# Kernel tuning notes

Measured on AMD Instinct MI355X. Metric: run time of the kernel, lower is better.

## Reference

```python
import jax, jax.numpy as jnp
import numpy as np

B = 256   # batch size; must equal N for the module's final broadcast to be valid
N = 256   # num feature vectors per sample
D = 1024  # feature dim
S = 1024  # state dim


def setup_inputs() -> dict:
    key = jax.random.key(0)
    k1, k2, k3, k4 = jax.random.split(key, 4)
    return {
        "feature_vectors": jax.random.normal(k1, (B, N, D), dtype=jnp.float32),
        "state_output": jax.random.normal(k2, (B, S), dtype=jnp.float32),
        # tf.random_normal_initializer default stddev=0.05
        "Q": 0.05 * jax.random.normal(k3, (S, S), dtype=jnp.float32),
        "K": 0.05 * jax.random.normal(k4, (S, N), dtype=jnp.float32),
    }


def reference(feature_vectors, state_output, Q, K):
    # Loop body: ((Q @ state^T)^T @ K) @ feature_vectors[i]
    # (Q @ state^T)^T == state @ Q^T  -> [B, S]
    A = state_output @ Q.T            # [B, S]
    M = A @ K                         # [B, N]
    # stack over i: W[i, b, d] = sum_n M[b, n] * FV[i, n, d]
    W = jnp.einsum('bn,ind->ibd', M, feature_vectors)   # [B, B, D]
    W = jax.nn.softmax(W, axis=-1)
    # broadcast multiply [B, B, D] * [B, N(=B), D], sum over axis=1
    context_vector = jnp.sum(W * feature_vectors, axis=1)  # [B, D]
    return (context_vector, W)
```

## Files before the change

### kernel.cpp

```cpp
#include <hip/hip_runtime.h>


typedef _Float16 half8 __attribute__((ext_vector_type(8)));
typedef _Float16 half4 __attribute__((ext_vector_type(4)));
typedef float floatx16 __attribute__((ext_vector_type(16)));

static __device__ __forceinline__ void split_f32(float x, _Float16& hi, _Float16& lo) {
    _Float16 h = (_Float16)x;
    hi = h;
    lo = (_Float16)(x - (float)h);
}

template <bool BT>
__global__ __launch_bounds__(256, 2) void gemm_splitk(
    const float* __restrict__ Ag, const float* __restrict__ Bg,
    float* __restrict__ Cf, int Kdim, int Ndim, int KC)
{
    __shared__ __align__(16) _Float16 AsHi[4 * 64 * 8];
    __shared__ __align__(16) _Float16 AsLo[4 * 64 * 8];
    __shared__ __align__(16) _Float16 BsHi[4 * 64 * 8];
    __shared__ __align__(16) _Float16 BsLo[4 * 64 * 8];

    const int tid  = threadIdx.x;
    const int lane = tid & 63;
    const int wave = tid >> 6;
    const int wy = wave >> 1, wx = wave & 1;
    const int l31 = lane & 31, l5 = lane >> 5;
    const int m0 = blockIdx.y * 64, n0 = blockIdx.x * 64;
    const int kt0 = (blockIdx.z * KC) >> 5;

    floatx16 acc;
#pragma unroll
    for (int j = 0; j < 16; ++j) acc[j] = 0.0f;

    const int sA_m  = tid >> 2;
    const int sA_kg = tid & 3;
    const int sB_n  = tid & 63;
    const int sB_kg = tid >> 6;

    const int nkt = KC / 32;
#pragma unroll 1
    for (int kt2 = 0; kt2 < nkt; ++kt2) {
        const int kt = kt0 + kt2;
        __syncthreads();
        {
            const float* src = Ag + (size_t)(m0 + sA_m) * Kdim + kt * 32 + sA_kg * 8;
            half8 hi, lo;
#pragma unroll
            for (int j = 0; j < 8; ++j) {
                _Float16 h, l;
                split_f32(src[j], h, l);
                hi[j] = h; lo[j] = l;
            }
            *(half8*)&AsHi[(sA_kg * 64 + sA_m) * 8] = hi;
            *(half8*)&AsLo[(sA_kg * 64 + sA_m) * 8] = lo;
        }
        if constexpr (BT) {
            const float* src = Bg + (size_t)(n0 + sA_m) * Kdim + kt * 32 + sA_kg * 8;
            half8 hi, lo;
#pragma unroll
            for (int j = 0; j < 8; ++j) {
                _Float16 h, l;
                split_f32(src[j], h, l);
                hi[j] = h; lo[j] = l;
            }
            *(half8*)&BsHi[(sA_kg * 64 + sA_m) * 8] = hi;
            *(half8*)&BsLo[(sA_kg * 64 + sA_m) * 8] = lo;
        } else {
            const float* src = Bg + (size_t)(kt * 32 + sB_kg * 8) * Ndim + n0 + sB_n;
            half8 hi, lo;
#pragma unroll
            for (int j = 0; j < 8; ++j) {
                _Float16 h, l;
                split_f32(src[(size_t)j * Ndim], h, l);
                hi[j] = h; lo[j] = l;
            }
            *(half8*)&BsHi[(sB_kg * 64 + sB_n) * 8] = hi;
            *(half8*)&BsLo[(sB_kg * 64 + sB_n) * 8] = lo;
        }
        __syncthreads();
#pragma unroll
        for (int ks = 0; ks < 2; ++ks) {
            const int kg = ks * 2 + l5;
            const half8 ah = *(half8*)&AsHi[(kg * 64 + wy * 32 + l31) * 8];
            const half8 al = *(half8*)&AsLo[(kg * 64 + wy * 32 + l31) * 8];
            const half8 bh = *(half8*)&BsHi[(kg * 64 + wx * 32 + l31) * 8];
            const half8 bl = *(half8*)&BsLo[(kg * 64 + wx * 32 + l31) * 8];
            acc = __builtin_amdgcn_mfma_f32_32x32x16_f16(ah, bh, acc, 0, 0, 0);
            acc = __builtin_amdgcn_mfma_f32_32x32x16_f16(ah, bl, acc, 0, 0, 0);
            acc = __builtin_amdgcn_mfma_f32_32x32x16_f16(al, bh, acc, 0, 0, 0);
        }
    }

#pragma unroll
    for (int reg = 0; reg < 16; ++reg) {
        const int row = m0 + wy * 32 + (reg & 3) + 8 * (reg >> 2) + 4 * l5;
        const int col = n0 + wx * 32 + l31;
        atomicAdd(&Cf[(size_t)row * Ndim + col], acc[reg]);
    }
}

static __device__ __forceinline__ int bs_swz(int byte_off) {
    return byte_off ^ (((byte_off >> 7) & 7) << 4);
}

__global__ __launch_bounds__(1024, 4) void fused_attn(
    const float* __restrict__ FV, const float* __restrict__ Mf,
    float* __restrict__ ctx, float* __restrict__ Wout)
{
    __shared__ __align__(16) _Float16 AsHi[2 * 64 * 8];
    __shared__ __align__(16) _Float16 AsLo[2 * 64 * 8];
    __shared__ __align__(16) _Float16 Bs[2 * 1024 * 8];
    __shared__ __align__(16) float red1[64 * 8];
    __shared__ __align__(16) float red2[64 * 8];

    const int tid  = threadIdx.x;
    const int lane = tid & 63;
    const int wave = tid >> 6;
    const int wx = wave & 7;
    const int wy = wave >> 3;
    const int l31 = lane & 31, l5 = lane >> 5;

    const int w   = blockIdx.x;
    const int xcd = w & 7;
    const int k   = w >> 3;
    const int i   = (xcd << 5) + (k >> 2);
    const int bt  = k & 3;

    const float* __restrict__ FVi = FV + (size_t)i * 256 * 1024;

    floatx16 acc[4];
#pragma unroll
    for (int nt = 0; nt < 4; ++nt)
#pragma unroll
        for (int j = 0; j < 16; ++j) acc[nt][j] = 0.0f;

    const int am = tid >> 1, akg = tid & 1;

    const int ng = tid >> 8;
    const int dq = tid & 255;

    float4 pv[4];
    float4 pa0, pa1;
#pragma unroll
    for (int r = 0; r < 4; ++r)
        pv[r] = *(const float4*)(FVi + (size_t)(ng * 4 + r) * 1024 + dq * 4);
    if (tid < 128) {
        const float* ap = Mf + (size_t)(bt * 64 + am) * 256 + akg * 8;
        pa0 = *(const float4*)(ap);
        pa1 = *(const float4*)(ap + 4);
    }

#pragma unroll 1
    for (int kt = 0; kt < 16; ++kt) {
        __syncthreads();
        if (tid < 128) {
            half8 hi, lo;
#pragma unroll
            for (int j = 0; j < 4; ++j) {
                _Float16 h, l;
                split_f32((&pa0.x)[j], h, l);
                hi[j] = h; lo[j] = l;
            }
#pragma unroll
            for (int j = 0; j < 4; ++j) {
                _Float16 h, l;
                split_f32((&pa1.x)[j], h, l);
                hi[4 + j] = h; lo[4 + j] = l;
            }
            *(half8*)&AsHi[(akg * 64 + am) * 8] = hi;
            *(half8*)&AsLo[(akg * 64 + am) * 8] = lo;
        }
#pragma unroll
        for (int j = 0; j < 4; ++j) {
            half4 h;
#pragma unroll
            for (int r = 0; r < 4; ++r) h[r] = (_Float16)((&pv[r].x)[j]);
            const int byte_off = ((ng >> 1) * 1024 + dq * 4 + j) * 16 + (ng & 1) * 8;
            *(half4*)((char*)Bs + bs_swz(byte_off)) = h;
        }
        __syncthreads();
        if (kt + 1 < 16) {
#pragma unroll
            for (int r = 0; r < 4; ++r)
                pv[r] = *(const float4*)(FVi + (size_t)((kt + 1) * 16 + ng * 4 + r) * 1024 + dq * 4);
            if (tid < 128) {
                const float* ap = Mf + (size_t)(bt * 64 + am) * 256 + (kt + 1) * 16 + akg * 8;
                pa0 = *(const float4*)(ap);
                pa1 = *(const float4*)(ap + 4);
            }
        }
        const half8 ah = *(half8*)&AsHi[(l5 * 64 + wy * 32 + l31) * 8];
        const half8 al = *(half8*)&AsLo[(l5 * 64 + wy * 32 + l31) * 8];
#pragma unroll
        for (int nt = 0; nt < 4; ++nt) {
            const int byte_off = (l5 * 1024 + wx * 128 + nt * 32 + l31) * 16;
            const half8 b = *(const half8*)((const char*)Bs + bs_swz(byte_off));
            acc[nt] = __builtin_amdgcn_mfma_f32_32x32x16_f16(ah, b, acc[nt], 0, 0, 0);
            acc[nt] = __builtin_amdgcn_mfma_f32_32x32x16_f16(al, b, acc[nt], 0, 0, 0);
        }
    }

#pragma unroll
    for (int reg = 0; reg < 16; ++reg) {
        float v = acc[0][reg];
#pragma unroll
        for (int nt = 1; nt < 4; ++nt) v = fmaxf(v, acc[nt][reg]);
#pragma unroll
        for (int off = 1; off < 32; off <<= 1) v = fmaxf(v, __shfl_xor(v, off));
        if (l31 == 0) {
            const int row = wy * 32 + (reg & 3) + 8 * (reg >> 2) + 4 * l5;
            red1[row * 8 + wx] = v;
        }
    }
    __syncthreads();
#pragma unroll
    for (int reg = 0; reg < 16; ++reg) {
        const int row = wy * 32 + (reg & 3) + 8 * (reg >> 2) + 4 * l5;
        const float4 a4 = *(const float4*)&red1[row * 8];
        const float4 b4 = *(const float4*)&red1[row * 8 + 4];
        const float rmax = fmaxf(fmaxf(fmaxf(a4.x, a4.y), fmaxf(a4.z, a4.w)),
                                 fmaxf(fmaxf(b4.x, b4.y), fmaxf(b4.z, b4.w)));
        float s = 0.0f;
#pragma unroll
        for (int nt = 0; nt < 4; ++nt) {
            const float p = __expf(acc[nt][reg] - rmax);
            acc[nt][reg] = p;
            s += p;
        }
#pragma unroll
        for (int off = 1; off < 32; off <<= 1) s += __shfl_xor(s, off);
        if (l31 == 0) red2[row * 8 + wx] = s;
    }
    __syncthreads();

    float csum[4];
#pragma unroll
    for (int nt = 0; nt < 4; ++nt) csum[nt] = 0.0f;

    const int rowbase = bt * 64 + wy * 32;
#pragma unroll
    for (int reg = 0; reg < 16; ++reg) {
        const int row = (reg & 3) + 8 * (reg >> 2) + 4 * l5;
        const float4 a4 = *(const float4*)&red2[(wy * 32 + row) * 8];
        const float4 b4 = *(const float4*)&red2[(wy * 32 + row) * 8 + 4];
        const float inv = 1.0f / (a4.x + a4.y + a4.z + a4.w + b4.x + b4.y + b4.z + b4.w);
#pragma unroll
        for (int nt = 0; nt < 4; ++nt) {
            const int col = wx * 128 + nt * 32 + l31;
            const float wv = acc[nt][reg] * inv;
            Wout[((size_t)(i * 256 + rowbase + row)) * 1024 + col] = wv;
            const float fv = FVi[(size_t)(rowbase + row) * 1024 + col];
            csum[nt] += wv * fv;
        }
    }
#pragma unroll
    for (int nt = 0; nt < 4; ++nt) {
        const float v = csum[nt] + __shfl_xor(csum[nt], 32);
        if (l5 == 0)
            atomicAdd(&ctx[(size_t)i * 1024 + wx * 128 + nt * 32 + l31], v);
    }
}

extern "C" void kernel_launch(void* const* d_in, const int* in_sizes, int n_in,
                              void* d_out, int out_size, void* d_ws, size_t ws_size,
                              hipStream_t stream)
{
    const float* FV    = (const float*)d_in[0];
    const float* state = (const float*)d_in[1];
    const float* Q     = (const float*)d_in[2];
    const float* Km    = (const float*)d_in[3];

    float* out = (float*)d_out;
    float* ctx = out;
    float* W   = out + 256 * 1024;

    char* ws = (char*)d_ws;
    float* A1 = (float*)ws;
    float* Mf = (float*)(ws + (1 << 20));

    (void)hipMemsetAsync(ws, 0, (1 << 20) + (1 << 18), stream);
    (void)hipMemsetAsync(ctx, 0, 256 * 1024 * sizeof(float), stream);

    gemm_splitk<true><<<dim3(16, 4, 8), 256, 0, stream>>>(
        state, Q, A1, 1024, 1024, 128);

    gemm_splitk<false><<<dim3(4, 4, 16), 256, 0, stream>>>(
        A1, Km, Mf, 1024, 256, 64);

    fused_attn<<<dim3(1024), 1024, 0, stream>>>(FV, Mf, ctx, W);
}
```

Measured before the change: 585.7 us.

## Split fused attention into two D-sliced passes with cross-slice softmax stats

Replaces the single fused kernel (one block per 64 rows over full D) with two launches where each block covers all 256 rows for a 256-wide D slice. Pass 1 computes per-slice row max and exp-sum into workspace. Pass 2 recomputes the GEMM, merges the slice statistics, and writes normalized W and the context sum using the FV slice cached in LDS. This cuts redundant FV reads and reuses the staged FV tile for the context product, but recomputes the GEMM and runs with large LDS and low occupancy.

After: 727.1 us. 1.24x slower.

```diff
diff --git a/kernel.cpp b/kernel.cpp
--- a/kernel.cpp
+++ b/kernel.cpp
@@ -2,7 +2,6 @@
 
 
 typedef _Float16 half8 __attribute__((ext_vector_type(8)));
-typedef _Float16 half4 __attribute__((ext_vector_type(4)));
 typedef float floatx16 __attribute__((ext_vector_type(16)));
 
 static __device__ __forceinline__ void split_f32(float x, _Float16& hi, _Float16& lo) {
@@ -100,165 +99,169 @@
     }
 }
 
-static __device__ __forceinline__ int bs_swz(int byte_off) {
-    return byte_off ^ (((byte_off >> 7) & 7) << 4);
-}
-
-__global__ __launch_bounds__(1024, 4) void fused_attn(
+static __device__ __forceinline__ int swz5(int byte_off) {
+    return byte_off ^ (((byte_off >> 9) & 31) << 4);
+}
+
+template <int PASS>
+__global__ __launch_bounds__(512, 1) void pass_k(
     const float* __restrict__ FV, const float* __restrict__ Mf,
+    float* __restrict__ Sm, float* __restrict__ Ss,
     float* __restrict__ ctx, float* __restrict__ Wout)
 {
-    __shared__ __align__(16) _Float16 AsHi[2 * 64 * 8];
-    __shared__ __align__(16) _Float16 AsLo[2 * 64 * 8];
-    __shared__ __align__(16) _Float16 Bs[2 * 1024 * 8];
-    __shared__ __align__(16) float red1[64 * 8];
-    __shared__ __align__(16) float red2[64 * 8];
+    __shared__ __align__(16) _Float16 Bs[256 * 256];
+    __shared__ __align__(16) float redm[256 * 2];
+    __shared__ __align__(16) float reds[256 * 2];
 
     const int tid  = threadIdx.x;
     const int lane = tid & 63;
     const int wave = tid >> 6;
-    const int wx = wave & 7;
-    const int wy = wave >> 3;
+    const int wy   = wave >> 1;
+    const int wx   = wave & 1;
     const int l31 = lane & 31, l5 = lane >> 5;
 
-    const int w   = blockIdx.x;
-    const int xcd = w & 7;
-    const int k   = w >> 3;
-    const int i   = (xcd << 5) + (k >> 2);
-    const int bt  = k & 3;
-
-    const float* __restrict__ FVi = FV + (size_t)i * 256 * 1024;
-
-    floatx16 acc[4];
-#pragma unroll
-    for (int nt = 0; nt < 4; ++nt)
-#pragma unroll
-        for (int j = 0; j < 16; ++j) acc[nt][j] = 0.0f;
-
-    const int am = tid >> 1, akg = tid & 1;
-
-    const int ng = tid >> 8;
-    const int dq = tid & 255;
-
-    float4 pv[4];
-    float4 pa0, pa1;
-#pragma unroll
-    for (int r = 0; r < 4; ++r)
-        pv[r] = *(const float4*)(FVi + (size_t)(ng * 4 + r) * 1024 + dq * 4);
-    if (tid < 128) {
-        const float* ap = Mf + (size_t)(bt * 64 + am) * 256 + akg * 8;
-        pa0 = *(const float4*)(ap);
-        pa1 = *(const float4*)(ap + 4);
-    }
+    const int i  = blockIdx.x >> 2;
+    const int ds = blockIdx.x & 3;
+
+    const float* __restrict__ FVi = FV + (size_t)i * 262144 + ds * 256;
+
+    floatx16 acc[8];
+#pragma unroll
+    for (int t = 0; t < 8; ++t)
+#pragma unroll
+        for (int j = 0; j < 16; ++j) acc[t][j] = 0.0f;
+
+    const int sd  = tid & 255;
+    const int snh = tid >> 8;
+
+    const float* __restrict__ Ar0 = Mf + (size_t)(wy * 64 + l31) * 256 + l5 * 8;
+    const float* __restrict__ Ar1 = Mf + (size_t)(wy * 64 + 32 + l31) * 256 + l5 * 8;
+
+    float pv[8];
+#pragma unroll
+    for (int r = 0; r < 8; ++r)
+        pv[r] = FVi[(size_t)(snh * 8 + r) * 1024 + sd];
 
 #pragma unroll 1
     for (int kt = 0; kt < 16; ++kt) {
-        __syncthreads();
-        if (tid < 128) {
-            half8 hi, lo;
+        {
+            half8 h;
+#pragma unroll
+            for (int r = 0; r < 8; ++r) h[r] = (_Float16)pv[r];
+            const int byte_off = sd * 512 + (kt * 16 + snh * 8) * 2;
+            *(half8*)((char*)Bs + swz5(byte_off)) = h;
+        }
+        __syncthreads();
+        if (kt + 1 < 16) {
+#pragma unroll
+            for (int r = 0; r < 8; ++r)
+                pv[r] = FVi[(size_t)((kt + 1) * 16 + snh * 8 + r) * 1024 + sd];
+        }
+        half8 ah0, al0, ah1, al1;
+        {
+            const float4 x0 = *(const float4*)(Ar0 + kt * 16);
+            const float4 x1 = *(const float4*)(Ar0 + kt * 16 + 4);
+            const float4 y0 = *(const float4*)(Ar1 + kt * 16);
+            const float4 y1 = *(const float4*)(Ar1 + kt * 16 + 4);
 #pragma unroll
             for (int j = 0; j < 4; ++j) {
                 _Float16 h, l;
-                split_f32((&pa0.x)[j], h, l);
-                hi[j] = h; lo[j] = l;
-            }
-#pragma unroll
-            for (int j = 0; j < 4; ++j) {
-                _Float16 h, l;
-                split_f32((&pa1.x)[j], h, l);
-                hi[4 + j] = h; lo[4 + j] = l;
-            }
-            *(half8*)&AsHi[(akg * 64 + am) * 8] = hi;
-            *(half8*)&AsLo[(akg * 64 + am) * 8] = lo;
-        }
-#pragma unroll
-        for (int j = 0; j < 4; ++j) {
-            half4 h;
-#pragma unroll
-            for (int r = 0; r < 4; ++r) h[r] = (_Float16)((&pv[r].x)[j]);
-            const int byte_off = ((ng >> 1) * 1024 + dq * 4 + j) * 16 + (ng & 1) * 8;
-            *(half4*)((char*)Bs + bs_swz(byte_off)) = h;
-        }
-        __syncthreads();
-        if (kt + 1 < 16) {
-#pragma unroll
-            for (int r = 0; r < 4; ++r)
-                pv[r] = *(const float4*)(FVi + (size_t)((kt + 1) * 16 + ng * 4 + r) * 1024 + dq * 4);
-            if (tid < 128) {
-                const float* ap = Mf + (size_t)(bt * 64 + am) * 256 + (kt + 1) * 16 + akg * 8;
-                pa0 = *(const float4*)(ap);
-                pa1 = *(const float4*)(ap + 4);
-            }
-        }
-        const half8 ah = *(half8*)&AsHi[(l5 * 64 + wy * 32 + l31) * 8];
-        const half8 al = *(half8*)&AsLo[(l5 * 64 + wy * 32 + l31) * 8];
-#pragma unroll
-        for (int nt = 0; nt < 4; ++nt) {
-            const int byte_off = (l5 * 1024 + wx * 128 + nt * 32 + l31) * 16;
-            const half8 b = *(const half8*)((const char*)Bs + bs_swz(byte_off));
-            acc[nt] = __builtin_amdgcn_mfma_f32_32x32x16_f16(ah, b, acc[nt], 0, 0, 0);
-            acc[nt] = __builtin_amdgcn_mfma_f32_32x32x16_f16(al, b, acc[nt], 0, 0, 0);
-        }
-    }
-
-#pragma unroll
-    for (int reg = 0; reg < 16; ++reg) {
-        float v = acc[0][reg];
-#pragma unroll
-        for (int nt = 1; nt < 4; ++nt) v = fmaxf(v, acc[nt][reg]);
-#pragma unroll
-        for (int off = 1; off < 32; off <<= 1) v = fmaxf(v, __shfl_xor(v, off));
-        if (l31 == 0) {
-            const int row = wy * 32 + (reg & 3) + 8 * (reg >> 2) + 4 * l5;
-            red1[row * 8 + wx] = v;
-        }
-    }
-    __syncthreads();
-#pragma unroll
-    for (int reg = 0; reg < 16; ++reg) {
-        const int row = wy * 32 + (reg & 3) + 8 * (reg >> 2) + 4 * l5;
-        const float4 a4 = *(const float4*)&red1[row * 8];
-        const float4 b4 = *(const float4*)&red1[row * 8 + 4];
-        const float rmax = fmaxf(fmaxf(fmaxf(a4.x, a4.y), fmaxf(a4.z, a4.w)),
-                                 fmaxf(fmaxf(b4.x, b4.y), fmaxf(b4.z, b4.w)));
-        float s = 0.0f;
-#pragma unroll
-        for (int nt = 0; nt < 4; ++nt) {
-            const float p = __expf(acc[nt][reg] - rmax);
-            acc[nt][reg] = p;
-            s += p;
-        }
-#pragma unroll
-        for (int off = 1; off < 32; off <<= 1) s += __shfl_xor(s, off);
-        if (l31 == 0) red2[row * 8 + wx] = s;
-    }
-    __syncthreads();
-
-    float csum[4];
-#pragma unroll
-    for (int nt = 0; nt < 4; ++nt) csum[nt] = 0.0f;
-
-    const int rowbase = bt * 64 + wy * 32;
-#pragma unroll
-    for (int reg = 0; reg < 16; ++reg) {
-        const int row = (reg & 3) + 8 * (reg >> 2) + 4 * l5;
-        const float4 a4 = *(const float4*)&red2[(wy * 32 + row) * 8];
-        const float4 b4 = *(const float4*)&red2[(wy * 32 + row) * 8 + 4];
-        const float inv = 1.0f / (a4.x + a4.y + a4.z + a4.w + b4.x + b4.y + b4.z + b4.w);
-#pragma unroll
-        for (int nt = 0; nt < 4; ++nt) {
-            const int col = wx * 128 + nt * 32 + l31;
-            const float wv = acc[nt][reg] * inv;
-            Wout[((size_t)(i * 256 + rowbase + row)) * 1024 + col] = wv;
-            const float fv = FVi[(size_t)(rowbase + row) * 1024 + col];
-            csum[nt] += wv * fv;
-        }
-    }
-#pragma unroll
-    for (int nt = 0; nt < 4; ++nt) {
-        const float v = csum[nt] + __shfl_xor(csum[nt], 32);
-        if (l5 == 0)
-            atomicAdd(&ctx[(size_t)i * 1024 + wx * 128 + nt * 32 + l31], v);
+                split_f32((&x0.x)[j], h, l); ah0[j] = h;     al0[j] = l;
+                split_f32((&x1.x)[j], h, l); ah0[4 + j] = h; al0[4 + j] = l;
+                split_f32((&y0.x)[j], h, l); ah1[j] = h;     al1[j] = l;
+                split_f32((&y1.x)[j], h, l); ah1[4 + j] = h; al1[4 + j] = l;
+            }
+        }
+#pragma unroll
+        for (int dt = 0; dt < 4; ++dt) {
+            const int byte_off = (wx * 128 + dt * 32 + l31) * 512 + (kt * 16 + l5 * 8) * 2;
+            const half8 b = *(const half8*)((const char*)Bs + swz5(byte_off));
+            acc[dt]     = __builtin_amdgcn_mfma_f32_32x32x16_f16(ah0, b, acc[dt], 0, 0, 0);
+            acc[dt]     = __builtin_amdgcn_mfma_f32_32x32x16_f16(al0, b, acc[dt], 0, 0, 0);
+            acc[4 + dt] = __builtin_amdgcn_mfma_f32_32x32x16_f16(ah1, b, acc[4 + dt], 0, 0, 0);
+            acc[4 + dt] = __builtin_amdgcn_mfma_f32_32x32x16_f16(al1, b, acc[4 + dt], 0, 0, 0);
+        }
+    }
+
+    if constexpr (PASS == 1) {
+#pragma unroll
+        for (int mt = 0; mt < 2; ++mt)
+#pragma unroll
+            for (int reg = 0; reg < 16; ++reg) {
+                float v = fmaxf(fmaxf(acc[mt * 4 + 0][reg], acc[mt * 4 + 1][reg]),
+                                fmaxf(acc[mt * 4 + 2][reg], acc[mt * 4 + 3][reg]));
+#pragma unroll
+                for (int off = 1; off < 32; off <<= 1) v = fmaxf(v, __shfl_xor(v, off));
+                if (l31 == 0) {
+                    const int row = wy * 64 + mt * 32 + (reg & 3) + 8 * (reg >> 2) + 4 * l5;
+                    redm[row * 2 + wx] = v;
+                }
+            }
+        __syncthreads();
+#pragma unroll
+        for (int mt = 0; mt < 2; ++mt)
+#pragma unroll
+            for (int reg = 0; reg < 16; ++reg) {
+                const int row = wy * 64 + mt * 32 + (reg & 3) + 8 * (reg >> 2) + 4 * l5;
+                const float m = fmaxf(redm[row * 2], redm[row * 2 + 1]);
+                float s = 0.0f;
+#pragma unroll
+                for (int dt = 0; dt < 4; ++dt) s += __expf(acc[mt * 4 + dt][reg] - m);
+#pragma unroll
+                for (int off = 1; off < 32; off <<= 1) s += __shfl_xor(s, off);
+                if (l31 == 0) reds[row * 2 + wx] = s;
+            }
+        __syncthreads();
+        if (tid < 256) {
+            const int b = tid;
+            const float m = fmaxf(redm[b * 2], redm[b * 2 + 1]);
+            const float s = reds[b * 2] + reds[b * 2 + 1];
+            const int sidx = (i * 4 + ds) * 256 + b;
+            Sm[sidx] = m;
+            Ss[sidx] = s;
+        }
+    } else {
+        if (tid < 256) {
+            const int b = tid;
+            float pm[4], ps[4];
+            float m = -3.0e38f;
+#pragma unroll
+            for (int p = 0; p < 4; ++p) {
+                pm[p] = Sm[(i * 4 + p) * 256 + b];
+                ps[p] = Ss[(i * 4 + p) * 256 + b];
+                m = fmaxf(m, pm[p]);
+            }
+            float S = 0.0f;
+#pragma unroll
+            for (int p = 0; p < 4; ++p) S += ps[p] * __expf(pm[p] - m);
+            redm[b] = m;
+            reds[b] = 1.0f / S;
+        }
+        __syncthreads();
+#pragma unroll
+        for (int dt = 0; dt < 4; ++dt) {
+            const int dloc  = wx * 128 + dt * 32 + l31;
+            const int dbyte = dloc * 512;
+            float csum = 0.0f;
+#pragma unroll
+            for (int mt = 0; mt < 2; ++mt)
+#pragma unroll
+                for (int no = 0; no < 4; ++no) {
+                    const half8 f = *(const half8*)((const char*)Bs +
+                        swz5(dbyte + (wy * 64 + mt * 32 + no * 8) * 2));
+#pragma unroll
+                    for (int rq = 0; rq < 4; ++rq) {
+                        const int reg = no * 4 + rq;
+                        const int row = wy * 64 + mt * 32 + rq + 8 * no + 4 * l5;
+                        const float wv = __expf(acc[mt * 4 + dt][reg] - redm[row]) * reds[row];
+                        Wout[((size_t)(i * 256 + row)) * 1024 + ds * 256 + dloc] = wv;
+                        csum += wv * (float)f[rq + 4 * l5];
+                    }
+                }
+            const float v = csum + __shfl_xor(csum, 32);
+            if (l5 == 0)
+                atomicAdd(&ctx[(size_t)i * 1024 + ds * 256 + dloc], v);
+        }
     }
 }
 
@@ -278,6 +281,8 @@
     char* ws = (char*)d_ws;
     float* A1 = (float*)ws;
     float* Mf = (float*)(ws + (1 << 20));
+    float* Sm = (float*)(ws + (1 << 20) + (1 << 18));
+    float* Ss = (float*)(ws + (2 << 20) + (1 << 18));
 
     (void)hipMemsetAsync(ws, 0, (1 << 20) + (1 << 18), stream);
     (void)hipMemsetAsync(ctx, 0, 256 * 1024 * sizeof(float), stream);
@@ -288,5 +293,7 @@
     gemm_splitk<false><<<dim3(4, 4, 16), 256, 0, stream>>>(
         A1, Km, Mf, 1024, 256, 64);
 
-    fused_attn<<<dim3(1024), 1024, 0, stream>>>(FV, Mf, ctx, W);
-}
+    pass_k<1><<<dim3(1024), 512, 0, stream>>>(FV, Mf, Sm, Ss, ctx, W);
+
+    pass_k<2><<<dim3(1024), 512, 0, stream>>>(FV, Mf, Sm, Ss, ctx, W);
+}
```
